# Kernel optimization log

Measured on AMD Instinct MI355X. Metric: run time of the kernel, lower is better.

The kernel has to match this reference:

```python
import jax, jax.numpy as jnp
import numpy as np

N_NODES = 20000
N_EDGES = 320000
C = 256
N_GRAPHS = 64
ADD_TO_EDGE_SCORE = 0.5


def setup_inputs() -> dict:
    key = jax.random.key(0)
    k1, k2, k3, k4 = jax.random.split(key, 4)
    x = jax.random.normal(k1, (N_NODES, C), jnp.float32)
    edge_index = jax.random.randint(k2, (2, N_EDGES), 0, N_NODES, dtype=jnp.int32)
    batch = jnp.sort(jax.random.randint(k3, (N_NODES,), 0, N_GRAPHS, dtype=jnp.int32))
    # Linear(2*C, 1) parameters
    lin_w = jax.random.normal(k4, (2 * C,), jnp.float32) / np.sqrt(2 * C)
    lin_b = jnp.zeros((), jnp.float32)
    return {"x": x, "edge_index": edge_index, "batch": batch, "lin_w": lin_w, "lin_b": lin_b}


def _edge_pool(x, edge_index, batch, lin_w, lin_b):
    N = x.shape[0]
    src, dst = edge_index[0], edge_index[1]
    # edge score: Linear(concat(x_src, x_dst)) done as two GEMVs to avoid [E,2C] concat
    e = x[src] @ lin_w[:C] + x[dst] @ lin_w[C:] + lin_b  # [E]
    e = jnp.tanh(e) + ADD_TO_EDGE_SCORE

    order = jnp.argsort(-e)  # descending score, greedy order
    s_s, d_s = src[order], dst[order]

    # sequential greedy maximal matching over sorted edges (int-only carry)
    def step(carry, sd):
        avail, cluster, i = carry
        s, d = sd
        take = avail[s] & avail[d]
        si = jnp.where(take, s, N)  # N is out-of-bounds sentinel -> dropped
        di = jnp.where(take, d, N)
        cluster = cluster.at[si].set(i, mode='drop').at[di].set(i, mode='drop')
        avail = avail.at[si].set(False, mode='drop').at[di].set(False, mode='drop')
        return (avail, cluster, i + take.astype(jnp.int32)), (take, i)

    init = (jnp.ones((N,), bool), jnp.zeros((N,), jnp.int32), jnp.int32(0))
    (avail, cluster, n_matched), (take_e, id_e) = jax.lax.scan(step, init, (s_s, d_s))

    # unmatched nodes become singleton clusters, in node-index order
    cluster = jnp.where(avail, n_matched + jnp.cumsum(avail.astype(jnp.int32)) - 1, cluster)
    num_clusters = n_matched + jnp.sum(avail.astype(jnp.int32))

    # per-cluster score: matched clusters get their edge score, singletons get 1.0
    cscore = jnp.ones((N,), x.dtype).at[jnp.where(take_e, id_e, N)].set(e[order], mode='drop')

    # scatter_add pooling then scale by cluster score (padded to N clusters; rows >= num_clusters are zero)
    new_x = jax.ops.segment_sum(x, cluster, num_segments=N) * cscore[:, None]
    new_edge_index = cluster[edge_index]  # remapped edges (coalesce dedup omitted: dynamic shape)
    new_batch = jnp.zeros((N,), batch.dtype).at[cluster].set(batch)
    return new_x, new_edge_index, cluster, new_batch, num_clusters


def reference(x, edge_index, batch, lin_w, lin_b):
    return _edge_pool(x, edge_index, batch, lin_w, lin_b)
```

## Files before the change

### kernel.cpp

```cpp
#include <hip/hip_runtime.h>

#define N_NODES 20000
#define N_EDGES 320000
#define CDIM    256
#define BE      1024
#define NBLK    313
#define NBN     20
#define CH      8192
#define NGRP    (CH/64)
#define NCH     ((N_EDGES + CH - 1) / CH)

#define OFF_X   0
#define OFF_EI  (N_NODES*CDIM)
#define OFF_CL  (OFF_EI + 2*N_EDGES)
#define OFF_B   (OFF_CL + N_NODES)
#define OFF_NC  (OFF_B + N_NODES)

__device__ __forceinline__ float xla_tanh(float x) {
  float ax = fabsf(x);
  float xc = fminf(fmaxf(x, -9.0f), 9.0f);
  float x2 = __fmul_rn(xc, xc);
  float p = -2.76076847742355e-16f;
  p = __fadd_rn(__fmul_rn(p, x2), 2.00018790482477e-13f);
  p = __fadd_rn(__fmul_rn(p, x2), -8.60467152213735e-11f);
  p = __fadd_rn(__fmul_rn(p, x2), 5.12229709037114e-08f);
  p = __fadd_rn(__fmul_rn(p, x2), 1.48572235717979e-05f);
  p = __fadd_rn(__fmul_rn(p, x2), 6.37261928875436e-04f);
  p = __fadd_rn(__fmul_rn(p, x2), 4.89352455891786e-03f);
  float num = __fmul_rn(xc, p);
  float q = 1.19825839466702e-06f;
  q = __fadd_rn(__fmul_rn(q, x2), 1.18534705686654e-04f);
  q = __fadd_rn(__fmul_rn(q, x2), 2.26843463243900e-03f);
  q = __fadd_rn(__fmul_rn(q, x2), 4.89352518554385e-03f);
  float r = num / q;
  return (ax < 0.0004f) ? x : r;
}

__global__ void k_node_dots(const float* __restrict__ x, const float* __restrict__ w,
                            float* __restrict__ p1, float* __restrict__ p2) {
  __shared__ float sw[2*CDIM];
  for (int i = threadIdx.x; i < 2*CDIM; i += blockDim.x) sw[i] = w[i];
  __syncthreads();
  int n = blockIdx.x * blockDim.x + threadIdx.x;
  if (n >= N_NODES) return;
  const float* row = x + (size_t)n * CDIM;
  float a1 = 0.f, a2 = 0.f;
  for (int k = 0; k < CDIM; ++k) {
    float xv = row[k];
    a1 = __fadd_rn(a1, __fmul_rn(xv, sw[k]));
    a2 = __fadd_rn(a2, __fmul_rn(xv, sw[CDIM + k]));
  }
  p1[n] = a1; p2[n] = a2;
}

__global__ void k_edge_scores(const int* __restrict__ ei, const float* __restrict__ p1,
                              const float* __restrict__ p2, const float* __restrict__ lb,
                              float* __restrict__ e, unsigned* __restrict__ keyA,
                              int* __restrict__ payA) {
  int i = blockIdx.x * blockDim.x + threadIdx.x;
  if (i >= N_EDGES) return;
  int s = ei[i], d = ei[N_EDGES + i];
  float z = __fadd_rn(__fadd_rn(p1[s], p2[d]), lb[0]);
  float ev = __fadd_rn(xla_tanh(z), 0.5f);
  e[i] = ev;
  unsigned u = __float_as_uint(ev);
  u = (u >> 31) ? ~u : (u | 0x80000000u);
  keyA[i] = ~u;
  payA[i] = i;
}

__global__ void k_radix_hist(const unsigned* __restrict__ key, int n, int shift,
                             unsigned* __restrict__ hist) {
  __shared__ unsigned h[256];
  int t = threadIdx.x;
  h[t] = 0;
  __syncthreads();
  int base = blockIdx.x * BE;
  for (int j = t; j < BE; j += 256) {
    int idx = base + j;
    if (idx < n) atomicAdd(&h[(key[idx] >> shift) & 255u], 1u);
  }
  __syncthreads();
  hist[t * NBLK + blockIdx.x] = h[t];
}

__global__ void k_radix_scan(unsigned* __restrict__ hist) {
  __shared__ unsigned sums[256];
  int t = threadIdx.x;
  unsigned rs = 0;
  for (int b = 0; b < NBLK; ++b) rs += hist[t * NBLK + b];
  sums[t] = rs;
  __syncthreads();
  for (int off = 1; off < 256; off <<= 1) {
    unsigned u2 = (t >= off) ? sums[t - off] : 0u;
    __syncthreads();
    sums[t] += u2;
    __syncthreads();
  }
  unsigned run = sums[t] - rs;
  for (int b = 0; b < NBLK; ++b) {
    unsigned tmp = hist[t * NBLK + b];
    hist[t * NBLK + b] = run;
    run += tmp;
  }
}

__global__ void k_radix_scatter(const unsigned* __restrict__ key, const int* __restrict__ pay,
                                int n, int shift, const unsigned* __restrict__ hist,
                                unsigned* __restrict__ keyo, int* __restrict__ payo) {
  __shared__ unsigned mask[256][8];
  __shared__ unsigned rbase[256];
  int t = threadIdx.x;
  rbase[t] = hist[t * NBLK + blockIdx.x];
  __syncthreads();
  int base = blockIdx.x * BE;
  for (int tile = 0; tile < BE / 256; ++tile) {
    for (int wq = 0; wq < 8; ++wq) mask[t][wq] = 0u;
    __syncthreads();
    int idx = base + tile * 256 + t;
    unsigned k = 0; int bin = 0; int valid = (idx < n);
    if (valid) {
      k = key[idx];
      bin = (k >> shift) & 255;
      atomicOr(&mask[bin][t >> 5], 1u << (t & 31));
    }
    __syncthreads();
    if (valid) {
      int w = t >> 5;
      unsigned r = 0;
      for (int w2 = 0; w2 < w; ++w2) r += __popc(mask[bin][w2]);
      r += __popc(mask[bin][w] & ((1u << (t & 31)) - 1u));
      unsigned pos = rbase[bin] + r;
      keyo[pos] = k;
      payo[pos] = pay[idx];
    }
    __syncthreads();
    unsigned c = 0;
    for (int wq = 0; wq < 8; ++wq) c += __popc(mask[t][wq]);
    rbase[t] += c;
    __syncthreads();
  }
}

__global__ void k_gather_sorted(const int* __restrict__ pay, const int* __restrict__ ei,
                                int* __restrict__ ss, int* __restrict__ dd,
                                unsigned long long* __restrict__ wl,
                                unsigned char* __restrict__ take) {
  int i = blockIdx.x * blockDim.x + threadIdx.x;
  if (i >= N_EDGES) return;
  int o = pay[i];
  int s = ei[o];
  int d = ei[N_EDGES + o];
  ss[i] = s;
  dd[i] = d;
  wl[i] = ((unsigned long long)i << 30) | ((unsigned long long)(unsigned)s << 15)
        | (unsigned long long)(unsigned)d;
  take[i] = 0;
}

__global__ __launch_bounds__(1024) void k_match(const unsigned long long* __restrict__ wl,
                                                unsigned char* __restrict__ take,
                                                int* __restrict__ g_avail) {
  __shared__ unsigned char avail[N_NODES];
  __shared__ unsigned long long comp[CH];
  __shared__ unsigned long long kmask[CH];
  __shared__ unsigned gcnt[NGRP];
  __shared__ unsigned gbase[NGRP];
  __shared__ int s_ncomp;
  int t = threadIdx.x;
  int lane = t & 63, wid = t >> 6;
  unsigned long long lmask_lt = (lane == 0) ? 0ull : (~0ull >> (64 - lane));
  for (int n = t; n < N_NODES; n += 1024) avail[n] = 1;
  __syncthreads();
  for (int c = 0; c < NCH; ++c) {
    int base = c * CH;
    unsigned long long myv[8];
    unsigned char myal[8];
    for (int it = 0; it < 8; ++it) {
      int rg = wid * 8 + it;
      int i = base + rg * 64 + lane;
      unsigned long long v = (i < N_EDGES) ? wl[i] : 0ull;
      bool a = false;
      if (i < N_EDGES) {
        int d = (int)(v & 0x7FFFu);
        int s = (int)((v >> 15) & 0x7FFFu);
        a = avail[s] && avail[d];
      }
      myv[it] = v; myal[it] = a ? 1 : 0;
      unsigned long long bal = __ballot(a);
      if (lane == 0) gcnt[rg] = (unsigned)__popcll(bal);
    }
    __syncthreads();
    if (wid == 0) {
      unsigned a0 = gcnt[lane], a1 = gcnt[64 + lane];
      unsigned s0 = a0;
      for (int o = 1; o < 64; o <<= 1) { unsigned u = __shfl_up(s0, o); if (lane >= o) s0 += u; }
      unsigned tot0 = __shfl(s0, 63);
      unsigned s1 = a1;
      for (int o = 1; o < 64; o <<= 1) { unsigned u = __shfl_up(s1, o); if (lane >= o) s1 += u; }
      gbase[lane] = s0 - a0;
      gbase[64 + lane] = tot0 + s1 - a1;
      if (lane == 63) s_ncomp = (int)(tot0 + s1);
    }
    __syncthreads();
    for (int it = 0; it < 8; ++it) {
      int rg = wid * 8 + it;
      unsigned long long bal = __ballot(myal[it] != 0);
      if (myal[it]) {
        unsigned r = (unsigned)__popcll(bal & lmask_lt);
        comp[gbase[rg] + r] = myv[it];
      }
    }
    __syncthreads();
    int ncomp = s_ncomp;
    for (int g = wid; g * 64 < ncomp; g += 16) {
      int i = g * 64 + lane;
      unsigned long long v = comp[i];
      int glen = ncomp - g * 64; if (glen > 64) glen = 64;
      int d = (int)(v & 0x7FFFu);
      int s = (int)((v >> 15) & 0x7FFFu);
      unsigned long long km = 1ull << lane;
      for (int j = 1; j < glen; ++j) {
        int sj = __builtin_amdgcn_readlane(s, j);
        int dj = __builtin_amdgcn_readlane(d, j);
        if (lane < j && (s == sj || s == dj || d == sj || d == dj))
          km |= 1ull << j;
      }
      kmask[i] = km;
    }
    __syncthreads();
    if (wid == 0) {
      int ncomp0 = s_ncomp;
      int ng = (ncomp0 + 63) >> 6;
      unsigned long long vcur = comp[lane];
      unsigned long long kcur = kmask[lane];
      for (int g = 0; g < ng; ++g) {
        int pi = ((g + 1) * 64 + lane) & (CH - 1);
        unsigned long long vnx = comp[pi];
        unsigned long long knx = kmask[pi];
        int glen = ncomp0 - g * 64; if (glen > 64) glen = 64;
        int d = (int)(vcur & 0x7FFFu);
        int s = (int)((vcur >> 15) & 0x7FFFu);
        unsigned km_lo = (unsigned)kcur;
        unsigned km_hi = (unsigned)(kcur >> 32);
        bool alive = (lane < glen) && avail[s] && avail[d];
        unsigned long long am = __ballot(alive);
        unsigned long long tk = 0;
        while (am) {
          int j = __ffsll((long long)am) - 1;
          tk |= 1ull << j;
          unsigned long long kj =
              ((unsigned long long)(unsigned)__builtin_amdgcn_readlane((int)km_hi, j) << 32)
            | (unsigned long long)(unsigned)__builtin_amdgcn_readlane((int)km_lo, j);
          am &= ~kj;
        }
        if ((tk >> lane) & 1ull) {
          take[(unsigned)(vcur >> 30)] = 1;
          avail[s] = 0; avail[d] = 0;
        }
        vcur = vnx; kcur = knx;
      }
    }
    __syncthreads();
  }
  for (int n = t; n < N_NODES; n += 1024) g_avail[n] = avail[n];
}

__global__ void k_parts(const unsigned char* __restrict__ take, const int* __restrict__ g_avail,
                        unsigned* __restrict__ tpart, unsigned* __restrict__ apart) {
  __shared__ unsigned s[256];
  int t = threadIdx.x;
  int b = blockIdx.x;
  unsigned c = 0;
  if (b < NBLK) {
    int base = b * BE;
    for (int j = t; j < BE; j += 256) { int idx = base + j; if (idx < N_EDGES) c += take[idx]; }
  } else {
    int base = (b - NBLK) * BE;
    for (int j = t; j < BE; j += 256) { int idx = base + j; if (idx < N_NODES) c += (unsigned)g_avail[idx]; }
  }
  s[t] = c; __syncthreads();
  for (int off = 128; off > 0; off >>= 1) { if (t < off) s[t] += s[t + off]; __syncthreads(); }
  if (t == 0) {
    if (b < NBLK) tpart[b] = s[0];
    else          apart[b - NBLK] = s[0];
  }
}

__global__ void k_scan_parts(unsigned* __restrict__ tpart, unsigned* __restrict__ apart,
                             int* __restrict__ scal) {
  __shared__ unsigned arr[512];
  int t = threadIdx.x;
  unsigned v = (t < NBLK) ? tpart[t] : 0u;
  arr[t] = v;
  __syncthreads();
  for (int off = 1; off < 512; off <<= 1) {
    unsigned u2 = (t >= off) ? arr[t - off] : 0u;
    __syncthreads();
    arr[t] += u2;
    __syncthreads();
  }
  unsigned excl = arr[t] - v;
  if (t < NBLK) tpart[t] = excl;
  unsigned nm = arr[511];
  __syncthreads();
  if (t == 0) {
    unsigned run = 0;
    for (int b = 0; b < NBN; ++b) { unsigned tmp = apart[b]; apart[b] = run; run += tmp; }
    scal[0] = (int)nm;
    scal[2] = (int)run;
    scal[1] = (int)(nm + run);
  }
}

__global__ void k_finalize_taken(const unsigned char* __restrict__ take, const int* __restrict__ pay,
                                 const int* __restrict__ ss, const int* __restrict__ dd,
                                 const float* __restrict__ e, const unsigned* __restrict__ tpart,
                                 int* __restrict__ cluster, int* __restrict__ clu,
                                 int* __restrict__ clv, float* __restrict__ csc) {
  __shared__ unsigned arr[256];
  int t = threadIdx.x; int b = blockIdx.x;
  int base = b * BE + t * 4;
  unsigned char tk[4];
  unsigned c = 0;
  for (int j = 0; j < 4; ++j) {
    int p = base + j;
    tk[j] = (p < N_EDGES) ? take[p] : (unsigned char)0;
    c += tk[j];
  }
  arr[t] = c;
  __syncthreads();
  unsigned v = c;
  for (int off = 1; off < 256; off <<= 1) {
    unsigned u2 = (t >= off) ? arr[t - off] : 0u;
    __syncthreads();
    arr[t] += u2;
    __syncthreads();
  }
  unsigned id = tpart[b] + (arr[t] - v);
  for (int j = 0; j < 4; ++j) {
    int p = base + j;
    if (p < N_EDGES && tk[j]) {
      int s = ss[p], d = dd[p];
      int u = min(s, d), w = max(s, d);
      cluster[s] = (int)id; cluster[d] = (int)id;
      clu[id] = u; clv[id] = w;
      csc[id] = e[pay[p]];
      ++id;
    }
  }
}

__global__ void k_finalize_single(const int* __restrict__ g_avail, const unsigned* __restrict__ apart,
                                  const int* __restrict__ scal, int* __restrict__ cluster,
                                  int* __restrict__ clu, int* __restrict__ clv,
                                  float* __restrict__ csc) {
  __shared__ unsigned arr[256];
  int t = threadIdx.x; int b = blockIdx.x;
  int base = b * BE + t * 4;
  unsigned char av[4];
  unsigned c = 0;
  for (int j = 0; j < 4; ++j) {
    int n = base + j;
    av[j] = (n < N_NODES) ? (unsigned char)g_avail[n] : (unsigned char)0;
    c += av[j];
  }
  arr[t] = c;
  __syncthreads();
  unsigned v = c;
  for (int off = 1; off < 256; off <<= 1) {
    unsigned u2 = (t >= off) ? arr[t - off] : 0u;
    __syncthreads();
    arr[t] += u2;
    __syncthreads();
  }
  unsigned id = (unsigned)scal[0] + apart[b] + (arr[t] - v);
  for (int j = 0; j < 4; ++j) {
    int n = base + j;
    if (n < N_NODES && av[j]) {
      cluster[n] = (int)id;
      clu[id] = n; clv[id] = n;
      csc[id] = 1.0f;
      ++id;
    }
  }
}

__global__ void k_out_x(const float* __restrict__ x, const int* __restrict__ clu,
                        const int* __restrict__ clv, const float* __restrict__ csc,
                        const int* __restrict__ scal, float* __restrict__ out) {
  int c = blockIdx.x; int t = threadIdx.x;
  int nc = scal[1];
  float v = 0.f;
  if (c < nc) {
    int u = clu[c], w = clv[c];
    float a = x[(size_t)u * CDIM + t];
    if (w != u) a = __fadd_rn(a, x[(size_t)w * CDIM + t]);
    v = __fmul_rn(a, csc[c]);
  }
  out[OFF_X + (size_t)c * CDIM + t] = v;
}

__global__ void k_out_edges(const int* __restrict__ ei, const int* __restrict__ cluster,
                            float* __restrict__ out) {
  int i = blockIdx.x * blockDim.x + threadIdx.x;
  if (i < 2 * N_EDGES) out[OFF_EI + i] = (float)cluster[ei[i]];
}

__global__ void k_out_rest(const int* __restrict__ cluster, const int* __restrict__ clv,
                           const int* __restrict__ batch, const int* __restrict__ scal,
                           float* __restrict__ out) {
  int i = blockIdx.x * blockDim.x + threadIdx.x;
  if (i >= N_NODES) return;
  int nc = scal[1];
  out[OFF_CL + i] = (float)cluster[i];
  out[OFF_B + i] = (i < nc) ? (float)batch[clv[i]] : 0.0f;
  if (i == 0) out[OFF_NC] = (float)nc;
}

extern "C" void kernel_launch(void* const* d_in, const int* in_sizes, int n_in,
                              void* d_out, int out_size, void* d_ws, size_t ws_size,
                              hipStream_t stream) {
  const float* x     = (const float*)d_in[0];
  const int*   ei    = (const int*)d_in[1];
  const int*   batch = (const int*)d_in[2];
  const float* lw    = (const float*)d_in[3];
  const float* lb    = (const float*)d_in[4];
  float* out = (float*)d_out;

  int* w = (int*)d_ws;
  size_t off = 0;
  auto alloc = [&](size_t n) { int* p = w + off; off += n; return p; };
  float*    p1    = (float*)alloc(N_NODES);
  float*    p2    = (float*)alloc(N_NODES);
  float*    e     = (float*)alloc(N_EDGES);
  unsigned* keyA  = (unsigned*)alloc(N_EDGES);
  unsigned* keyB  = (unsigned*)alloc(N_EDGES);
  int*      payA  = (int*)alloc(N_EDGES);
  int*      payB  = (int*)alloc(N_EDGES);
  unsigned* hist  = (unsigned*)alloc(256 * NBLK);
  off = (off + 1) & ~(size_t)1;
  unsigned long long* wl = (unsigned long long*)alloc(2 * N_EDGES);
  unsigned char* take = (unsigned char*)alloc(N_EDGES / 4);
  int*      cluster = (int*)alloc(N_NODES);
  int*      clu   = (int*)alloc(N_NODES);
  int*      clv   = (int*)alloc(N_NODES);
  float*    csc   = (float*)alloc(N_NODES);
  int*      g_avail = (int*)alloc(N_NODES);
  unsigned* tpart = (unsigned*)alloc(NBLK + 1);
  unsigned* apart = (unsigned*)alloc(NBN + 1);
  int*      scal  = (int*)alloc(16);
  int* ss = (int*)keyB;
  int* dd = payB;

  k_node_dots<<<(N_NODES + 255) / 256, 256, 0, stream>>>(x, lw, p1, p2);
  k_edge_scores<<<(N_EDGES + 255) / 256, 256, 0, stream>>>(ei, p1, p2, lb, e, keyA, payA);

  for (int pass = 0; pass < 4; ++pass) {
    int shift = pass * 8;
    const unsigned* ki = (pass & 1) ? keyB : keyA;
    unsigned*       ko = (pass & 1) ? keyA : keyB;
    const int*      pi = (pass & 1) ? payB : payA;
    int*            po = (pass & 1) ? payA : payB;
    k_radix_hist<<<NBLK, 256, 0, stream>>>(ki, N_EDGES, shift, hist);
    k_radix_scan<<<1, 256, 0, stream>>>(hist);
    k_radix_scatter<<<NBLK, 256, 0, stream>>>(ki, pi, N_EDGES, shift, hist, ko, po);
  }

  k_gather_sorted<<<(N_EDGES + 255) / 256, 256, 0, stream>>>(payA, ei, ss, dd, wl, take);
  k_match<<<1, 1024, 0, stream>>>(wl, take, g_avail);

  k_parts<<<NBLK + NBN, 256, 0, stream>>>(take, g_avail, tpart, apart);
  k_scan_parts<<<1, 512, 0, stream>>>(tpart, apart, scal);
  k_finalize_taken<<<NBLK, 256, 0, stream>>>(take, payA, ss, dd, e, tpart, cluster, clu, clv, csc);
  k_finalize_single<<<NBN, 256, 0, stream>>>(g_avail, apart, scal, cluster, clu, clv, csc);

  k_out_x<<<N_NODES, CDIM, 0, stream>>>(x, clu, clv, csc, scal, out);
  k_out_edges<<<(2 * N_EDGES + 255) / 256, 256, 0, stream>>>(ei, cluster, out);
  k_out_rest<<<(N_NODES + 255) / 256, 256, 0, stream>>>(cluster, clv, batch, scal, out);
}
```

Baseline: 1.159 ms.

## Fuse radix-sort stages, finalize and output kernels; pipeline greedy matching availability

Folds the first radix histogram into edge-score computation and the sorted gather into the last radix scatter. It also merges the two finalize kernels and the two small output kernels, cutting launches and global round trips. Inside the single-block matcher, the conflict mask is built from LDS loads rather than cross-lane readlane loops. The serial wave now prefetches availability for the next group, adjusting it against the edges just taken, so LDS load latency overlaps the greedy loop. The cost is extra workspace for separate ss/dd buffers and more complex matcher logic.

Result: slower. 1.844 ms (+59.2%).

```diff
diff --git a/kernel.cpp b/kernel.cpp
--- a/kernel.cpp
+++ b/kernel.cpp
@@ -53,20 +53,31 @@
   p1[n] = a1; p2[n] = a2;
 }
 
-__global__ void k_edge_scores(const int* __restrict__ ei, const float* __restrict__ p1,
-                              const float* __restrict__ p2, const float* __restrict__ lb,
-                              float* __restrict__ e, unsigned* __restrict__ keyA,
-                              int* __restrict__ payA) {
-  int i = blockIdx.x * blockDim.x + threadIdx.x;
-  if (i >= N_EDGES) return;
-  int s = ei[i], d = ei[N_EDGES + i];
-  float z = __fadd_rn(__fadd_rn(p1[s], p2[d]), lb[0]);
-  float ev = __fadd_rn(xla_tanh(z), 0.5f);
-  e[i] = ev;
-  unsigned u = __float_as_uint(ev);
-  u = (u >> 31) ? ~u : (u | 0x80000000u);
-  keyA[i] = ~u;
-  payA[i] = i;
+__global__ void k_edge_scores_hist(const int* __restrict__ ei, const float* __restrict__ p1,
+                                   const float* __restrict__ p2, const float* __restrict__ lb,
+                                   float* __restrict__ e, unsigned* __restrict__ keyA,
+                                   int* __restrict__ payA, unsigned* __restrict__ hist) {
+  __shared__ unsigned h[256];
+  int t = threadIdx.x;
+  h[t] = 0;
+  __syncthreads();
+  int base = blockIdx.x * BE;
+  for (int j = t; j < BE; j += 256) {
+    int i = base + j;
+    if (i >= N_EDGES) continue;
+    int s = ei[i], d = ei[N_EDGES + i];
+    float z = __fadd_rn(__fadd_rn(p1[s], p2[d]), lb[0]);
+    float ev = __fadd_rn(xla_tanh(z), 0.5f);
+    e[i] = ev;
+    unsigned u = __float_as_uint(ev);
+    u = (u >> 31) ? ~u : (u | 0x80000000u);
+    unsigned key = ~u;
+    keyA[i] = key;
+    payA[i] = i;
+    atomicAdd(&h[key & 255u], 1u);
+  }
+  __syncthreads();
+  hist[t * NBLK + blockIdx.x] = h[t];
 }
 
 __global__ void k_radix_hist(const unsigned* __restrict__ key, int n, int shift,
@@ -142,20 +153,51 @@
   }
 }
 
-__global__ void k_gather_sorted(const int* __restrict__ pay, const int* __restrict__ ei,
-                                int* __restrict__ ss, int* __restrict__ dd,
-                                unsigned long long* __restrict__ wl,
-                                unsigned char* __restrict__ take) {
-  int i = blockIdx.x * blockDim.x + threadIdx.x;
-  if (i >= N_EDGES) return;
-  int o = pay[i];
-  int s = ei[o];
-  int d = ei[N_EDGES + o];
-  ss[i] = s;
-  dd[i] = d;
-  wl[i] = ((unsigned long long)i << 30) | ((unsigned long long)(unsigned)s << 15)
-        | (unsigned long long)(unsigned)d;
-  take[i] = 0;
+__global__ void k_radix_scatter_final(const unsigned* __restrict__ key, const int* __restrict__ pay,
+                                      int n, int shift, const unsigned* __restrict__ hist,
+                                      const int* __restrict__ ei, int* __restrict__ payo,
+                                      int* __restrict__ ss, int* __restrict__ dd,
+                                      unsigned long long* __restrict__ wl,
+                                      unsigned char* __restrict__ take) {
+  __shared__ unsigned mask[256][8];
+  __shared__ unsigned rbase[256];
+  int t = threadIdx.x;
+  rbase[t] = hist[t * NBLK + blockIdx.x];
+  __syncthreads();
+  int base = blockIdx.x * BE;
+  for (int tile = 0; tile < BE / 256; ++tile) {
+    for (int wq = 0; wq < 8; ++wq) mask[t][wq] = 0u;
+    __syncthreads();
+    int idx = base + tile * 256 + t;
+    unsigned k = 0; int bin = 0; int valid = (idx < n);
+    if (valid) {
+      k = key[idx];
+      bin = (k >> shift) & 255;
+      atomicOr(&mask[bin][t >> 5], 1u << (t & 31));
+    }
+    __syncthreads();
+    if (valid) {
+      int w = t >> 5;
+      unsigned r = 0;
+      for (int w2 = 0; w2 < w; ++w2) r += __popc(mask[bin][w2]);
+      r += __popc(mask[bin][w] & ((1u << (t & 31)) - 1u));
+      unsigned pos = rbase[bin] + r;
+      int o = pay[idx];
+      int s = ei[o];
+      int d = ei[N_EDGES + o];
+      payo[pos] = o;
+      ss[pos] = s;
+      dd[pos] = d;
+      wl[pos] = ((unsigned long long)pos << 30) | ((unsigned long long)(unsigned)s << 15)
+              | (unsigned long long)(unsigned)d;
+      take[pos] = 0;
+    }
+    __syncthreads();
+    unsigned c = 0;
+    for (int wq = 0; wq < 8; ++wq) c += __popc(mask[t][wq]);
+    rbase[t] += c;
+    __syncthreads();
+  }
 }
 
 __global__ __launch_bounds__(1024) void k_match(const unsigned long long* __restrict__ wl,
@@ -215,50 +257,67 @@
     int ncomp = s_ncomp;
     for (int g = wid; g * 64 < ncomp; g += 16) {
       int i = g * 64 + lane;
-      unsigned long long v = comp[i];
-      int glen = ncomp - g * 64; if (glen > 64) glen = 64;
+      unsigned long long v = (i < ncomp) ? comp[i] : 0ull;
       int d = (int)(v & 0x7FFFu);
       int s = (int)((v >> 15) & 0x7FFFu);
       unsigned long long km = 1ull << lane;
-      for (int j = 1; j < glen; ++j) {
-        int sj = __builtin_amdgcn_readlane(s, j);
-        int dj = __builtin_amdgcn_readlane(d, j);
-        if (lane < j && (s == sj || s == dj || d == sj || d == dj))
-          km |= 1ull << j;
+      if (i < ncomp) {
+        int glen = ncomp - g * 64; if (glen > 64) glen = 64;
+        for (int j = lane + 1; j < glen; ++j) {
+          unsigned long long vj = comp[g * 64 + j];
+          int dj = (int)(vj & 0x7FFFu);
+          int sj = (int)((vj >> 15) & 0x7FFFu);
+          if (sj == s || sj == d || dj == s || dj == d) km |= 1ull << j;
+        }
       }
       kmask[i] = km;
     }
     __syncthreads();
     if (wid == 0) {
       int ncomp0 = s_ncomp;
-      int ng = (ncomp0 + 63) >> 6;
-      unsigned long long vcur = comp[lane];
-      unsigned long long kcur = kmask[lane];
-      for (int g = 0; g < ng; ++g) {
-        int pi = ((g + 1) * 64 + lane) & (CH - 1);
-        unsigned long long vnx = comp[pi];
-        unsigned long long knx = kmask[pi];
-        int glen = ncomp0 - g * 64; if (glen > 64) glen = 64;
-        int d = (int)(vcur & 0x7FFFu);
-        int s = (int)((vcur >> 15) & 0x7FFFu);
-        unsigned km_lo = (unsigned)kcur;
-        unsigned km_hi = (unsigned)(kcur >> 32);
-        bool alive = (lane < glen) && avail[s] && avail[d];
-        unsigned long long am = __ballot(alive);
-        unsigned long long tk = 0;
-        while (am) {
-          int j = __ffsll((long long)am) - 1;
-          tk |= 1ull << j;
-          unsigned long long kj =
-              ((unsigned long long)(unsigned)__builtin_amdgcn_readlane((int)km_hi, j) << 32)
-            | (unsigned long long)(unsigned)__builtin_amdgcn_readlane((int)km_lo, j);
-          am &= ~kj;
+      if (ncomp0 > 0) {
+        int ng = (ncomp0 + 63) >> 6;
+        unsigned long long vcur = comp[lane];
+        unsigned long long kcur = kmask[lane];
+        int sc = (int)((vcur >> 15) & 0x7FFFu);
+        int dc = (int)(vcur & 0x7FFFu);
+        int glen0 = ncomp0 < 64 ? ncomp0 : 64;
+        bool ac = (lane < glen0) && avail[sc] && avail[dc];
+        for (int g = 0; g < ng; ++g) {
+          int glen_n = ncomp0 - (g + 1) * 64; if (glen_n > 64) glen_n = 64;
+          int pi = ((g + 1) * 64 + lane) & (CH - 1);
+          unsigned long long vnx = comp[pi];
+          unsigned long long knx = kmask[pi];
+          int sn = (int)((vnx >> 15) & 0x7FFFu);
+          int dn = (int)(vnx & 0x7FFFu);
+          unsigned char a1 = avail[sn];
+          unsigned char a2 = avail[dn];
+          unsigned long long am = __ballot(ac);
+          unsigned km_lo = (unsigned)kcur, km_hi = (unsigned)(kcur >> 32);
+          unsigned long long tk = 0;
+          while (am) {
+            int j = __ffsll((long long)am) - 1;
+            tk |= 1ull << j;
+            unsigned long long kj =
+                ((unsigned long long)(unsigned)__builtin_amdgcn_readlane((int)km_hi, j) << 32)
+              | (unsigned long long)(unsigned)__builtin_amdgcn_readlane((int)km_lo, j);
+            am &= ~kj;
+          }
+          if ((tk >> lane) & 1ull) {
+            take[(unsigned)(vcur >> 30)] = 1;
+            avail[sc] = 0; avail[dc] = 0;
+          }
+          bool an = (glen_n > 0) && (lane < glen_n) && a1 && a2;
+          unsigned long long tkit = tk;
+          while (tkit) {
+            int j = __ffsll((long long)tkit) - 1;
+            tkit &= tkit - 1;
+            int sj = __builtin_amdgcn_readlane(sc, j);
+            int dj = __builtin_amdgcn_readlane(dc, j);
+            an = an && !(sn == sj || sn == dj || dn == sj || dn == dj);
+          }
+          vcur = vnx; kcur = knx; sc = sn; dc = dn; ac = an;
         }
-        if ((tk >> lane) & 1ull) {
-          take[(unsigned)(vcur >> 30)] = 1;
-          avail[s] = 0; avail[d] = 0;
-        }
-        vcur = vnx; kcur = knx;
       }
     }
     __syncthreads();
@@ -313,75 +372,73 @@
   }
 }
 
-__global__ void k_finalize_taken(const unsigned char* __restrict__ take, const int* __restrict__ pay,
-                                 const int* __restrict__ ss, const int* __restrict__ dd,
-                                 const float* __restrict__ e, const unsigned* __restrict__ tpart,
-                                 int* __restrict__ cluster, int* __restrict__ clu,
-                                 int* __restrict__ clv, float* __restrict__ csc) {
+__global__ void k_finalize(const unsigned char* __restrict__ take, const int* __restrict__ pay,
+                           const int* __restrict__ ss, const int* __restrict__ dd,
+                           const float* __restrict__ e, const unsigned* __restrict__ tpart,
+                           const int* __restrict__ g_avail, const unsigned* __restrict__ apart,
+                           const int* __restrict__ scal, int* __restrict__ cluster,
+                           int* __restrict__ clu, int* __restrict__ clv,
+                           float* __restrict__ csc) {
   __shared__ unsigned arr[256];
   int t = threadIdx.x; int b = blockIdx.x;
-  int base = b * BE + t * 4;
-  unsigned char tk[4];
-  unsigned c = 0;
-  for (int j = 0; j < 4; ++j) {
-    int p = base + j;
-    tk[j] = (p < N_EDGES) ? take[p] : (unsigned char)0;
-    c += tk[j];
-  }
-  arr[t] = c;
-  __syncthreads();
-  unsigned v = c;
-  for (int off = 1; off < 256; off <<= 1) {
-    unsigned u2 = (t >= off) ? arr[t - off] : 0u;
-    __syncthreads();
-    arr[t] += u2;
-    __syncthreads();
-  }
-  unsigned id = tpart[b] + (arr[t] - v);
-  for (int j = 0; j < 4; ++j) {
-    int p = base + j;
-    if (p < N_EDGES && tk[j]) {
-      int s = ss[p], d = dd[p];
-      int u = min(s, d), w = max(s, d);
-      cluster[s] = (int)id; cluster[d] = (int)id;
-      clu[id] = u; clv[id] = w;
-      csc[id] = e[pay[p]];
-      ++id;
-    }
-  }
-}
-
-__global__ void k_finalize_single(const int* __restrict__ g_avail, const unsigned* __restrict__ apart,
-                                  const int* __restrict__ scal, int* __restrict__ cluster,
-                                  int* __restrict__ clu, int* __restrict__ clv,
-                                  float* __restrict__ csc) {
-  __shared__ unsigned arr[256];
-  int t = threadIdx.x; int b = blockIdx.x;
-  int base = b * BE + t * 4;
-  unsigned char av[4];
-  unsigned c = 0;
-  for (int j = 0; j < 4; ++j) {
-    int n = base + j;
-    av[j] = (n < N_NODES) ? (unsigned char)g_avail[n] : (unsigned char)0;
-    c += av[j];
-  }
-  arr[t] = c;
-  __syncthreads();
-  unsigned v = c;
-  for (int off = 1; off < 256; off <<= 1) {
-    unsigned u2 = (t >= off) ? arr[t - off] : 0u;
-    __syncthreads();
-    arr[t] += u2;
-    __syncthreads();
-  }
-  unsigned id = (unsigned)scal[0] + apart[b] + (arr[t] - v);
-  for (int j = 0; j < 4; ++j) {
-    int n = base + j;
-    if (n < N_NODES && av[j]) {
-      cluster[n] = (int)id;
-      clu[id] = n; clv[id] = n;
-      csc[id] = 1.0f;
-      ++id;
+  if (b < NBLK) {
+    int base = b * BE + t * 4;
+    unsigned char tk[4];
+    unsigned c = 0;
+    for (int j = 0; j < 4; ++j) {
+      int p = base + j;
+      tk[j] = (p < N_EDGES) ? take[p] : (unsigned char)0;
+      c += tk[j];
+    }
+    arr[t] = c;
+    __syncthreads();
+    unsigned v = c;
+    for (int off = 1; off < 256; off <<= 1) {
+      unsigned u2 = (t >= off) ? arr[t - off] : 0u;
+      __syncthreads();
+      arr[t] += u2;
+      __syncthreads();
+    }
+    unsigned id = tpart[b] + (arr[t] - v);
+    for (int j = 0; j < 4; ++j) {
+      int p = base + j;
+      if (p < N_EDGES && tk[j]) {
+        int s = ss[p], d = dd[p];
+        int u = min(s, d), w = max(s, d);
+        cluster[s] = (int)id; cluster[d] = (int)id;
+        clu[id] = u; clv[id] = w;
+        csc[id] = e[pay[p]];
+        ++id;
+      }
+    }
+  } else {
+    int bb = b - NBLK;
+    int base = bb * BE + t * 4;
+    unsigned char av[4];
+    unsigned c = 0;
+    for (int j = 0; j < 4; ++j) {
+      int n = base + j;
+      av[j] = (n < N_NODES) ? (unsigned char)g_avail[n] : (unsigned char)0;
+      c += av[j];
+    }
+    arr[t] = c;
+    __syncthreads();
+    unsigned v = c;
+    for (int off = 1; off < 256; off <<= 1) {
+      unsigned u2 = (t >= off) ? arr[t - off] : 0u;
+      __syncthreads();
+      arr[t] += u2;
+      __syncthreads();
+    }
+    unsigned id = (unsigned)scal[0] + apart[bb] + (arr[t] - v);
+    for (int j = 0; j < 4; ++j) {
+      int n = base + j;
+      if (n < N_NODES && av[j]) {
+        cluster[n] = (int)id;
+        clu[id] = n; clv[id] = n;
+        csc[id] = 1.0f;
+        ++id;
+      }
     }
   }
 }
@@ -401,21 +458,17 @@
   out[OFF_X + (size_t)c * CDIM + t] = v;
 }
 
-__global__ void k_out_edges(const int* __restrict__ ei, const int* __restrict__ cluster,
-                            float* __restrict__ out) {
+__global__ void k_out_er(const int* __restrict__ ei, const int* __restrict__ cluster,
+                         const int* __restrict__ clv, const int* __restrict__ batch,
+                         const int* __restrict__ scal, float* __restrict__ out) {
   int i = blockIdx.x * blockDim.x + threadIdx.x;
   if (i < 2 * N_EDGES) out[OFF_EI + i] = (float)cluster[ei[i]];
-}
-
-__global__ void k_out_rest(const int* __restrict__ cluster, const int* __restrict__ clv,
-                           const int* __restrict__ batch, const int* __restrict__ scal,
-                           float* __restrict__ out) {
-  int i = blockIdx.x * blockDim.x + threadIdx.x;
-  if (i >= N_NODES) return;
-  int nc = scal[1];
-  out[OFF_CL + i] = (float)cluster[i];
-  out[OFF_B + i] = (i < nc) ? (float)batch[clv[i]] : 0.0f;
-  if (i == 0) out[OFF_NC] = (float)nc;
+  if (i < N_NODES) {
+    int nc = scal[1];
+    out[OFF_CL + i] = (float)cluster[i];
+    out[OFF_B + i] = (i < nc) ? (float)batch[clv[i]] : 0.0f;
+    if (i == 0) out[OFF_NC] = (float)nc;
+  }
 }
 
 extern "C" void kernel_launch(void* const* d_in, const int* in_sizes, int n_in,
@@ -438,6 +491,8 @@
   unsigned* keyB  = (unsigned*)alloc(N_EDGES);
   int*      payA  = (int*)alloc(N_EDGES);
   int*      payB  = (int*)alloc(N_EDGES);
+  int*      ss    = (int*)alloc(N_EDGES);
+  int*      dd    = (int*)alloc(N_EDGES);
   unsigned* hist  = (unsigned*)alloc(256 * NBLK);
   off = (off + 1) & ~(size_t)1;
   unsigned long long* wl = (unsigned long long*)alloc(2 * N_EDGES);
@@ -450,32 +505,30 @@
   unsigned* tpart = (unsigned*)alloc(NBLK + 1);
   unsigned* apart = (unsigned*)alloc(NBN + 1);
   int*      scal  = (int*)alloc(16);
-  int* ss = (int*)keyB;
-  int* dd = payB;
 
   k_node_dots<<<(N_NODES + 255) / 256, 256, 0, stream>>>(x, lw, p1, p2);
-  k_edge_scores<<<(N_EDGES + 255) / 256, 256, 0, stream>>>(ei, p1, p2, lb, e, keyA, payA);
-
-  for (int pass = 0; pass < 4; ++pass) {
-    int shift = pass * 8;
-    const unsigned* ki = (pass & 1) ? keyB : keyA;
-    unsigned*       ko = (pass & 1) ? keyA : keyB;
-    const int*      pi = (pass & 1) ? payB : payA;
-    int*            po = (pass & 1) ? payA : payB;
-    k_radix_hist<<<NBLK, 256, 0, stream>>>(ki, N_EDGES, shift, hist);
-    k_radix_scan<<<1, 256, 0, stream>>>(hist);
-    k_radix_scatter<<<NBLK, 256, 0, stream>>>(ki, pi, N_EDGES, shift, hist, ko, po);
-  }
-
-  k_gather_sorted<<<(N_EDGES + 255) / 256, 256, 0, stream>>>(payA, ei, ss, dd, wl, take);
+  k_edge_scores_hist<<<NBLK, 256, 0, stream>>>(ei, p1, p2, lb, e, keyA, payA, hist);
+
+  k_radix_scan<<<1, 256, 0, stream>>>(hist);
+  k_radix_scatter<<<NBLK, 256, 0, stream>>>(keyA, payA, N_EDGES, 0, hist, keyB, payB);
+  k_radix_hist<<<NBLK, 256, 0, stream>>>(keyB, N_EDGES, 8, hist);
+  k_radix_scan<<<1, 256, 0, stream>>>(hist);
+  k_radix_scatter<<<NBLK, 256, 0, stream>>>(keyB, payB, N_EDGES, 8, hist, keyA, payA);
+  k_radix_hist<<<NBLK, 256, 0, stream>>>(keyA, N_EDGES, 16, hist);
+  k_radix_scan<<<1, 256, 0, stream>>>(hist);
+  k_radix_scatter<<<NBLK, 256, 0, stream>>>(keyA, payA, N_EDGES, 16, hist, keyB, payB);
+  k_radix_hist<<<NBLK, 256, 0, stream>>>(keyB, N_EDGES, 24, hist);
+  k_radix_scan<<<1, 256, 0, stream>>>(hist);
+  k_radix_scatter_final<<<NBLK, 256, 0, stream>>>(keyB, payB, N_EDGES, 24, hist, ei,
+                                                  payA, ss, dd, wl, take);
+
   k_match<<<1, 1024, 0, stream>>>(wl, take, g_avail);
 
   k_parts<<<NBLK + NBN, 256, 0, stream>>>(take, g_avail, tpart, apart);
   k_scan_parts<<<1, 512, 0, stream>>>(tpart, apart, scal);
-  k_finalize_taken<<<NBLK, 256, 0, stream>>>(take, payA, ss, dd, e, tpart, cluster, clu, clv, csc);
-  k_finalize_single<<<NBN, 256, 0, stream>>>(g_avail, apart, scal, cluster, clu, clv, csc);
+  k_finalize<<<NBLK + NBN, 256, 0, stream>>>(take, payA, ss, dd, e, tpart,
+                                             g_avail, apart, scal, cluster, clu, clv, csc);
 
   k_out_x<<<N_NODES, CDIM, 0, stream>>>(x, clu, clv, csc, scal, out);
-  k_out_edges<<<(2 * N_EDGES + 255) / 256, 256, 0, stream>>>(ei, cluster, out);
-  k_out_rest<<<(N_NODES + 255) / 256, 256, 0, stream>>>(cluster, clv, batch, scal, out);
-}
+  k_out_er<<<(2 * N_EDGES + 255) / 256, 256, 0, stream>>>(ei, cluster, clv, batch, scal, out);
+}
```
